# Optimization experiments

Hardware: AMD Instinct MI355X
Metric: run time of the kernel (lower is better)

Reference implementation:

```python
import jax, jax.numpy as jnp
import numpy as np

Q = 8192      # num query tokens
S = 32768     # num support points
E = 131072    # num edges (query<-support neighbor pairs)
D = 256       # token_dim
H = 8         # num_heads
HD = D // H   # head_dim = 32
GEO = 128     # geo mlp_hidden = geo_dim
FFN = 2 * D   # ffn hidden
STAT_IN = 12  # 4 stats * 3 coords
EPS_LN = 1e-5


def gelu(x):
    return jax.nn.gelu(x, approximate=False)  # torch nn.GELU default (erf)


def layernorm(x, g, b):
    m = jnp.mean(x, axis=-1, keepdims=True)
    v = jnp.mean((x - m) ** 2, axis=-1, keepdims=True)
    return (x - m) * jax.lax.rsqrt(v + EPS_LN) * g + b


def setup_inputs() -> dict:
    key = jax.random.key(0)
    ks = jax.random.split(key, 16)
    w = lambda k, shp: jax.random.normal(k, shp, jnp.float32) * 0.02
    return {
        "query_tokens": jax.random.normal(ks[0], (Q, D), jnp.float32),
        "query_pos": jax.random.normal(ks[1], (Q, 3), jnp.float32),
        "support_feats": jax.random.normal(ks[2], (S, D), jnp.float32),
        "support_pos": jax.random.normal(ks[3], (S, 3), jnp.float32),
        "Wq": w(ks[4], (D, D)), "Wk": w(ks[5], (D, D)), "Wv": w(ks[6], (D, D)),
        "Wg": w(ks[7], (GEO, D)),
        "Wo": w(ks[8], (D, D)), "bo": jnp.zeros((D,), jnp.float32),
        "log_tau": jnp.array(0.0, jnp.float32),
        "ln1_g": jnp.ones((D,), jnp.float32), "ln1_b": jnp.zeros((D,), jnp.float32),
        "ln2_g": jnp.ones((D,), jnp.float32), "ln2_b": jnp.zeros((D,), jnp.float32),
        "Wf1": w(ks[9], (D, FFN)), "bf1": jnp.zeros((FFN,), jnp.float32),
        "Wf2": w(ks[10], (FFN, D)), "bf2": jnp.zeros((D,), jnp.float32),
        "Gw1": w(ks[11], (STAT_IN, GEO)), "Gb1": jnp.zeros((GEO,), jnp.float32),
        "Gw2": w(ks[12], (GEO, GEO)), "Gb2": jnp.zeros((GEO,), jnp.float32),
        "q_idx": jnp.sort(jax.random.randint(ks[13], (E,), 0, Q)),
        "s_idx": jax.random.randint(ks[14], (E,), 0, S),
        "num_queries": Q,
    }


def geo_stats(rel, q_idx, num_q):
    # rel: [E,3] relative positions; segmented mean/std/min/max -> [num_q, 12]
    ones = jnp.ones((rel.shape[0], 1), rel.dtype)
    cnt = jnp.maximum(jax.ops.segment_sum(ones, q_idx, num_q), 1.0)  # [Q,1]
    mean = jax.ops.segment_sum(rel, q_idx, num_q) / cnt
    var = jax.ops.segment_sum((rel - mean[q_idx]) ** 2, q_idx, num_q) / cnt
    std = jnp.sqrt(var)
    # torch inits min/max with +/-inf then clamps to [-100,100]; jax segment
    # min/max init with dtype extremes -> same result after clip
    mn = jnp.clip(jax.ops.segment_min(rel, q_idx, num_q), -100.0, 100.0)
    mx = jnp.clip(jax.ops.segment_max(rel, q_idx, num_q), -100.0, 100.0)
    return jnp.concatenate([mean, std, mn, mx], axis=-1)


def reference(query_tokens, query_pos, support_feats, support_pos,
              Wq, Wk, Wv, Wg, Wo, bo, log_tau,
              ln1_g, ln1_b, ln2_g, ln2_b,
              Wf1, bf1, Wf2, bf2, Gw1, Gb1, Gw2, Gb2,
              q_idx, s_idx, num_queries):
    num_q = num_queries
    # ---- statistical geo embedding ----
    rel = support_pos[s_idx] - query_pos[q_idx]                 # [E,3]
    raw = geo_stats(rel, q_idx, num_q)                          # [Q,12]
    geo = gelu(gelu(raw @ Gw1 + Gb1) @ Gw2 + Gb2)               # [Q,GEO]

    # ---- AGNO cross attention (pre-norm) ----
    qt = layernorm(query_tokens, ln1_g, ln1_b)
    Qf = qt @ Wq                                                # [Q,D]
    Kf = support_feats @ Wk                                     # [S,D]
    Vf = support_feats @ Wv                                     # [S,D]
    Gf = geo @ Wg                                               # [Q,D]
    qh = Qf[q_idx].reshape(E, H, HD)
    kh = Kf[s_idx].reshape(E, H, HD)
    vh = Vf[s_idx].reshape(E, H, HD)
    gh = Gf[q_idx].reshape(E, H, HD)
    tau = jnp.exp(log_tau)
    scores = jnp.sum(qh * kh, axis=-1) / (jnp.sqrt(jnp.float32(HD)) * tau)  # [E,H]
    # torch scores_max starts at 0 -> max(0, segment max)
    smax = jnp.maximum(jax.ops.segment_max(scores, q_idx, num_q), 0.0)
    ex = jnp.exp(scores - smax[q_idx])
    ssum = jax.ops.segment_sum(ex, q_idx, num_q)
    alpha = ex / jnp.maximum(ssum[q_idx], 1e-8)                 # [E,H]
    weighted = alpha[..., None] * (vh + gh)                     # [E,H,HD]
    out = jax.ops.segment_sum(weighted, q_idx, num_q)           # [Q,H,HD]
    attn = out.reshape(num_q, D) @ Wo + bo

    # ---- residual + FFN ----
    x = query_tokens + attn
    x = x + gelu(layernorm(x, ln2_g, ln2_b) @ Wf1 + bf1) @ Wf2 + bf2
    return x
```

## Files before the change

kernel.cpp:

```cpp
#include <hip/hip_runtime.h>
#include <math.h>

#define QN 8192
#define SN 32768
#define EN 131072
#define DN 256
#define HN 8
#define HDN 32
#define GEON 128
#define FFNN 512

typedef __attribute__((ext_vector_type(8))) short bf16x8;
typedef __attribute__((ext_vector_type(8))) unsigned short u16x8;
typedef __attribute__((ext_vector_type(4))) unsigned short u16x4;
typedef __attribute__((ext_vector_type(4))) float f32x4;

__device__ __forceinline__ unsigned short f2b(float f) {
  union { float f; unsigned u; } v; v.f = f;
  unsigned u = v.u;
  u += 0x7fffu + ((u >> 16) & 1u);
  return (unsigned short)(u >> 16);
}
__device__ __forceinline__ float b2f(unsigned short h) {
  union { unsigned u; float f; } v; v.u = ((unsigned)h) << 16; return v.f;
}
__device__ __forceinline__ float gelu_f(float x) {
  return 0.5f * x * (1.0f + erff(x * 0.70710678118654752440f));
}

__global__ __launch_bounds__(256) void transpose_weights(
    const float* Wq, const float* Wk, const float* Wv, const float* Wg,
    const float* Wo, const float* Wf1, const float* Wf2,
    unsigned short* WqT, unsigned short* WkvT, unsigned short* WgT,
    unsigned short* WoT, unsigned short* Wf1T, unsigned short* Wf2T) {
  int b = blockIdx.x;
  const float* src; unsigned short* dst; int K, N, tile;
  if (b < 16)       { src = Wq;  dst = WqT;          K = 256; N = 256; tile = b; }
  else if (b < 32)  { src = Wk;  dst = WkvT;         K = 256; N = 256; tile = b - 16; }
  else if (b < 48)  { src = Wv;  dst = WkvT + 65536; K = 256; N = 256; tile = b - 32; }
  else if (b < 56)  { src = Wg;  dst = WgT;          K = 128; N = 256; tile = b - 48; }
  else if (b < 72)  { src = Wo;  dst = WoT;          K = 256; N = 256; tile = b - 56; }
  else if (b < 104) { src = Wf1; dst = Wf1T;         K = 256; N = 512; tile = b - 72; }
  else              { src = Wf2; dst = Wf2T;         K = 512; N = 256; tile = b - 104; }
  int ktiles = K >> 6;
  int k0 = (tile % ktiles) * 64, n0 = (tile / ktiles) * 64;
  __shared__ float ts[64][65];
  int t = threadIdx.x;
  int c4 = (t & 15) * 4;
  int r = t >> 4;
#pragma unroll
  for (int p = 0; p < 4; ++p) {
    int row = p * 16 + r;
    float4 v = *(const float4*)(src + (size_t)(k0 + row) * N + n0 + c4);
    ts[row][c4 + 0] = v.x; ts[row][c4 + 1] = v.y;
    ts[row][c4 + 2] = v.z; ts[row][c4 + 3] = v.w;
  }
  __syncthreads();
#pragma unroll
  for (int p = 0; p < 4; ++p) {
    int n = p * 16 + r;
    ushort4 o;
    o.x = f2b(ts[c4 + 0][n]); o.y = f2b(ts[c4 + 1][n]);
    o.z = f2b(ts[c4 + 2][n]); o.w = f2b(ts[c4 + 3][n]);
    *(ushort4*)(dst + (size_t)(n0 + n) * K + k0 + c4) = o;
  }
}

__global__ __launch_bounds__(256) void seg_offsets(const int* q_idx, int* offs) {
  int i = blockIdx.x * 256 + threadIdx.x;
  if (i > QN) return;
  int lo = 0, hi = EN;
  while (lo < hi) {
    int mid = (lo + hi) >> 1;
    if (q_idx[mid] < i) lo = mid + 1; else hi = mid;
  }
  offs[i] = lo;
}

__global__ __launch_bounds__(256) void geo_stats_kernel(
    const float* qpos, const float* spos, const int* offs, const int* s_idx, float* raw) {
  int q = blockIdx.x * 64 + (threadIdx.x >> 2);
  int sub = threadIdx.x & 3;
  int e0 = offs[q], e1 = offs[q + 1];
  float qx = qpos[q * 3 + 0], qy = qpos[q * 3 + 1], qz = qpos[q * 3 + 2];
  float cnt = 0.f, sx = 0.f, sy = 0.f, sz = 0.f, sxx = 0.f, syy = 0.f, szz = 0.f;
  float mnx = 1e30f, mny = 1e30f, mnz = 1e30f, mxx = -1e30f, mxy = -1e30f, mxz = -1e30f;
  for (int e = e0 + sub; e < e1; e += 4) {
    int s = s_idx[e];
    float rx = spos[s * 3 + 0] - qx;
    float ry = spos[s * 3 + 1] - qy;
    float rz = spos[s * 3 + 2] - qz;
    cnt += 1.f;
    sx += rx; sy += ry; sz += rz;
    sxx += rx * rx; syy += ry * ry; szz += rz * rz;
    mnx = fminf(mnx, rx); mny = fminf(mny, ry); mnz = fminf(mnz, rz);
    mxx = fmaxf(mxx, rx); mxy = fmaxf(mxy, ry); mxz = fmaxf(mxz, rz);
  }
#pragma unroll
  for (int msk = 1; msk <= 2; msk <<= 1) {
    cnt += __shfl_xor(cnt, msk);
    sx += __shfl_xor(sx, msk); sy += __shfl_xor(sy, msk); sz += __shfl_xor(sz, msk);
    sxx += __shfl_xor(sxx, msk); syy += __shfl_xor(syy, msk); szz += __shfl_xor(szz, msk);
    mnx = fminf(mnx, __shfl_xor(mnx, msk));
    mny = fminf(mny, __shfl_xor(mny, msk));
    mnz = fminf(mnz, __shfl_xor(mnz, msk));
    mxx = fmaxf(mxx, __shfl_xor(mxx, msk));
    mxy = fmaxf(mxy, __shfl_xor(mxy, msk));
    mxz = fmaxf(mxz, __shfl_xor(mxz, msk));
  }
  if (sub == 0) {
    float c = fmaxf(cnt, 1.f);
    float mx_ = sx / c, my_ = sy / c, mz_ = sz / c;
    float vx = fmaxf(sxx / c - mx_ * mx_, 0.f);
    float vy = fmaxf(syy / c - my_ * my_, 0.f);
    float vz = fmaxf(szz / c - mz_ * mz_, 0.f);
    float* r = raw + (size_t)q * 12;
    r[0] = mx_; r[1] = my_; r[2] = mz_;
    r[3] = sqrtf(vx); r[4] = sqrtf(vy); r[5] = sqrtf(vz);
    r[6] = fminf(fmaxf(mnx, -100.f), 100.f);
    r[7] = fminf(fmaxf(mny, -100.f), 100.f);
    r[8] = fminf(fmaxf(mnz, -100.f), 100.f);
    r[9] = fminf(fmaxf(mxx, -100.f), 100.f);
    r[10] = fminf(fmaxf(mxy, -100.f), 100.f);
    r[11] = fminf(fmaxf(mxz, -100.f), 100.f);
  }
}

__global__ __launch_bounds__(128) void geo_mlp_kernel(
    const float* raw, const float* Gw1, const float* Gb1,
    const float* Gw2, const float* Gb2, unsigned short* geo_b) {
  int qb = blockIdx.x * 8;
  int j = threadIdx.x;
  __shared__ float rs[8][12];
  __shared__ float h1[8][128];
  if (j < 96) rs[j / 12][j % 12] = raw[(size_t)(qb + j / 12) * 12 + (j % 12)];
  __syncthreads();
  float b1 = Gb1[j];
  float acc[8];
#pragma unroll
  for (int qq = 0; qq < 8; ++qq) acc[qq] = b1;
  for (int i = 0; i < 12; ++i) {
    float w = Gw1[i * GEON + j];
#pragma unroll
    for (int qq = 0; qq < 8; ++qq) acc[qq] += rs[qq][i] * w;
  }
#pragma unroll
  for (int qq = 0; qq < 8; ++qq) h1[qq][j] = gelu_f(acc[qq]);
  __syncthreads();
  float b2 = Gb2[j];
  float acc2[8];
#pragma unroll
  for (int qq = 0; qq < 8; ++qq) acc2[qq] = b2;
  for (int k = 0; k < 128; ++k) {
    float w = Gw2[k * GEON + j];
#pragma unroll
    for (int qq = 0; qq < 8; ++qq) acc2[qq] += h1[qq][k] * w;
  }
#pragma unroll
  for (int qq = 0; qq < 8; ++qq)
    geo_b[(size_t)(qb + qq) * GEON + j] = f2b(gelu_f(acc2[qq]));
}

__global__ __launch_bounds__(256) void ln_kernel(
    const float* x, const float* g, const float* b, unsigned short* out) {
  int row = blockIdx.x * 4 + (threadIdx.x >> 6);
  int lane = threadIdx.x & 63;
  const float* xr = x + (size_t)row * DN;
  float4 v = *(const float4*)(xr + lane * 4);
  float s = v.x + v.y + v.z + v.w;
  float ss = v.x * v.x + v.y * v.y + v.z * v.z + v.w * v.w;
#pragma unroll
  for (int msk = 1; msk <= 32; msk <<= 1) {
    s += __shfl_xor(s, msk);
    ss += __shfl_xor(ss, msk);
  }
  float mean = s * (1.f / 256.f);
  float var = ss * (1.f / 256.f) - mean * mean;
  float rs = 1.0f / sqrtf(var + 1e-5f);
  float4 gg = *(const float4*)(g + lane * 4);
  float4 bb = *(const float4*)(b + lane * 4);
  unsigned short* o = out + (size_t)row * DN + lane * 4;
  o[0] = f2b((v.x - mean) * rs * gg.x + bb.x);
  o[1] = f2b((v.y - mean) * rs * gg.y + bb.y);
  o[2] = f2b((v.z - mean) * rs * gg.z + bb.z);
  o[3] = f2b((v.w - mean) * rs * gg.w + bb.w);
}

__device__ __forceinline__ u16x8* lds_g(unsigned short* base, int row, int col) {
  int g = (col >> 3) ^ (row & 7);
  return reinterpret_cast<u16x8*>(base + row * 256 + g * 8);
}
__global__ __launch_bounds__(256) void kv_gemm(
    const float* A, const unsigned short* BT, unsigned short* KVb) {
  __shared__ unsigned short As[64 * 256];
  __shared__ unsigned short Bs[32 * 256];
  int t = threadIdx.x;
  int bm = blockIdx.x * 64;
  int w = t >> 6, lane = t & 63;
  int quad = lane >> 4, l16 = lane & 15;
  int wr = w >> 1, wc = w & 1;
  int srow = t >> 2, sub = t & 3;
  {
    const float* Ag = A + (size_t)(bm + srow) * 256 + sub * 64;
#pragma unroll
    for (int i = 0; i < 8; ++i) {
      float4 f0 = *(const float4*)(Ag + i * 8);
      float4 f1 = *(const float4*)(Ag + i * 8 + 4);
      u16x8 u;
      u[0] = f2b(f0.x); u[1] = f2b(f0.y); u[2] = f2b(f0.z); u[3] = f2b(f0.w);
      u[4] = f2b(f1.x); u[5] = f2b(f1.y); u[6] = f2b(f1.z); u[7] = f2b(f1.w);
      *lds_g(As, srow, sub * 64 + i * 8) = u;
    }
  }
  int brow = t >> 3, bsub = t & 7;
  for (int ct = 0; ct < 16; ++ct) {
    {
      const unsigned short* Bg = BT + (size_t)(ct * 32 + brow) * 256 + bsub * 32;
#pragma unroll
      for (int i = 0; i < 4; ++i)
        *lds_g(Bs, brow, bsub * 32 + i * 8) = *reinterpret_cast<const u16x8*>(Bg + i * 8);
    }
    __syncthreads();
    f32x4 acc[2];
    acc[0] = (f32x4){0.f, 0.f, 0.f, 0.f};
    acc[1] = (f32x4){0.f, 0.f, 0.f, 0.f};
#pragma unroll
    for (int k = 0; k < 8; ++k) {
      bf16x8 a0 = *reinterpret_cast<bf16x8*>(lds_g(As, wr * 32 + l16, k * 32 + quad * 8));
      bf16x8 a1 = *reinterpret_cast<bf16x8*>(lds_g(As, wr * 32 + 16 + l16, k * 32 + quad * 8));
      bf16x8 b0 = *reinterpret_cast<bf16x8*>(lds_g(Bs, wc * 16 + l16, k * 32 + quad * 8));
      acc[0] = __builtin_amdgcn_mfma_f32_16x16x32_bf16(a0, b0, acc[0], 0, 0, 0);
      acc[1] = __builtin_amdgcn_mfma_f32_16x16x32_bf16(a1, b0, acc[1], 0, 0, 0);
    }
#pragma unroll
    for (int i = 0; i < 2; ++i)
#pragma unroll
      for (int r = 0; r < 4; ++r) {
        int rw = bm + wr * 32 + i * 16 + quad * 4 + r;
        int col = ct * 32 + wc * 16 + l16;
        KVb[(size_t)rw * 512 + col] = f2b(acc[i][r]);
      }
    __syncthreads();
  }
}

template <bool A_FP32, bool COLGRID, bool HAS_BIAS, bool DO_GELU, bool HAS_RESID, bool STORE_F32>
__global__ __launch_bounds__(256) void gemm64(
    const void* Ap, const unsigned short* BT, int M, int N, int K,
    const float* bias, const float* resid, float* outF, unsigned short* outB) {
  __shared__ unsigned short As[64][40];
  __shared__ unsigned short Bs[64][40];
  int t = threadIdx.x;
  int bm = (COLGRID ? blockIdx.x : blockIdx.y) * 64;
  int bn = (COLGRID ? blockIdx.y : blockIdx.x) * 64;
  int w = t >> 6, lane = t & 63;
  int wr = w >> 1, wc = w & 1;
  int quad = lane >> 4, l16 = lane & 15;
  int row = t >> 2, chunk = t & 3;

  f32x4 acc[2][2];
#pragma unroll
  for (int i = 0; i < 2; ++i)
#pragma unroll
    for (int j = 0; j < 2; ++j) acc[i][j] = (f32x4){0.f, 0.f, 0.f, 0.f};

  for (int k0 = 0; k0 < K; k0 += 32) {
    if (A_FP32) {
      const float* Ag = (const float*)Ap + (size_t)(bm + row) * K + k0 + chunk * 8;
      float4 f0 = *(const float4*)Ag;
      float4 f1 = *(const float4*)(Ag + 4);
      u16x8 u;
      u[0] = f2b(f0.x); u[1] = f2b(f0.y); u[2] = f2b(f0.z); u[3] = f2b(f0.w);
      u[4] = f2b(f1.x); u[5] = f2b(f1.y); u[6] = f2b(f1.z); u[7] = f2b(f1.w);
      *reinterpret_cast<u16x8*>(&As[row][chunk * 8]) = u;
    } else {
      const unsigned short* Ag = (const unsigned short*)Ap + (size_t)(bm + row) * K + k0 + chunk * 8;
      *reinterpret_cast<u16x8*>(&As[row][chunk * 8]) = *reinterpret_cast<const u16x8*>(Ag);
    }
    {
      const unsigned short* Bg = BT + (size_t)(bn + row) * K + k0 + chunk * 8;
      *reinterpret_cast<u16x8*>(&Bs[row][chunk * 8]) = *reinterpret_cast<const u16x8*>(Bg);
    }
    __syncthreads();
    bf16x8 a0 = *reinterpret_cast<const bf16x8*>(&As[wr * 32 + l16][quad * 8]);
    bf16x8 a1 = *reinterpret_cast<const bf16x8*>(&As[wr * 32 + 16 + l16][quad * 8]);
    bf16x8 b0 = *reinterpret_cast<const bf16x8*>(&Bs[wc * 32 + l16][quad * 8]);
    bf16x8 b1 = *reinterpret_cast<const bf16x8*>(&Bs[wc * 32 + 16 + l16][quad * 8]);
    acc[0][0] = __builtin_amdgcn_mfma_f32_16x16x32_bf16(a0, b0, acc[0][0], 0, 0, 0);
    acc[0][1] = __builtin_amdgcn_mfma_f32_16x16x32_bf16(a0, b1, acc[0][1], 0, 0, 0);
    acc[1][0] = __builtin_amdgcn_mfma_f32_16x16x32_bf16(a1, b0, acc[1][0], 0, 0, 0);
    acc[1][1] = __builtin_amdgcn_mfma_f32_16x16x32_bf16(a1, b1, acc[1][1], 0, 0, 0);
    __syncthreads();
  }

#pragma unroll
  for (int i = 0; i < 2; ++i)
#pragma unroll
    for (int j = 0; j < 2; ++j) {
      int col = bn + wc * 32 + j * 16 + l16;
      float bv = HAS_BIAS ? bias[col] : 0.f;
#pragma unroll
      for (int r = 0; r < 4; ++r) {
        int rw = bm + wr * 32 + i * 16 + quad * 4 + r;
        float v = acc[i][j][r] + bv;
        if (DO_GELU) v = gelu_f(v);
        if (HAS_RESID) v += resid[(size_t)rw * N + col];
        if (STORE_F32) outF[(size_t)rw * N + col] = v;
        else outB[(size_t)rw * N + col] = f2b(v);
      }
    }
}

__global__ __launch_bounds__(256) void attn_edge_kernel(
    const unsigned short* Qb, const unsigned short* Gfb, const unsigned short* KVb,
    const int* s_idx, const int* offs, const float* log_tau, unsigned short* attn_b) {
  int q = blockIdx.x * 4 + (threadIdx.x >> 6);
  int lane = threadIdx.x & 63;
  int half = lane >> 5;
  int sl = lane & 31;
  int d0 = sl * 8;
  int e0 = offs[q], e1 = offs[q + 1];
  float invs = expf(-log_tau[0]) * 0.17677669529663687f;
  u16x8 qu = *(const u16x8*)(Qb + (size_t)q * DN + d0);
  u16x8 gu = *(const u16x8*)(Gfb + (size_t)q * DN + d0);
  float qf[8], gf[8];
#pragma unroll
  for (int j = 0; j < 8; ++j) { qf[j] = b2f(qu[j]) * invs; gf[j] = b2f(gu[j]); }
  const float NEG = -1e30f;
  float m = -INFINITY, l = 0.f;
  float a[8];
#pragma unroll
  for (int j = 0; j < 8; ++j) a[j] = 0.f;
  for (int e = e0; e < e1; e += 2) {
    int ee = e + half;
    bool valid = ee < e1;
    int s = s_idx[valid ? ee : (e1 - 1)];
    const unsigned short* kr = KVb + (size_t)s * 512 + d0;
    u16x8 ku = *(const u16x8*)kr;
    u16x8 vu = *(const u16x8*)(kr + 256);
    float p = 0.f;
#pragma unroll
    for (int j = 0; j < 8; ++j) p += qf[j] * b2f(ku[j]);
    p += __shfl_xor(p, 1);
    p += __shfl_xor(p, 2);
    if (!valid) p = -INFINITY;
    float mnew = fmaxf(m, p);
    float sc = (m > NEG) ? __expf(m - mnew) : 0.f;
    float we = valid ? __expf(p - mnew) : 0.f;
    l = l * sc + we;
#pragma unroll
    for (int j = 0; j < 8; ++j) a[j] = a[j] * sc + we * (b2f(vu[j]) + gf[j]);
    m = mnew;
  }
  float om = __shfl_xor(m, 32);
  float ol = __shfl_xor(l, 32);
  float M2 = fmaxf(m, om);
  float ws = (m > NEG) ? __expf(m - M2) : 0.f;
  float wo = (om > NEG) ? __expf(om - M2) : 0.f;
  l = l * ws + ol * wo;
#pragma unroll
  for (int j = 0; j < 8; ++j) {
    float oa = __shfl_xor(a[j], 32);
    a[j] = a[j] * ws + oa * wo;
  }
  float M = fmaxf(M2, 0.f);
  float em = (M2 > NEG) ? __expf(M2 - M) : 0.f;
  float denom = fmaxf(l * em, 1e-8f);
  float f = em / denom;
  if (half == 0) {
    u16x8 o;
#pragma unroll
    for (int j = 0; j < 8; ++j) o[j] = f2b(a[j] * f);
    *(u16x8*)(attn_b + (size_t)q * DN + d0) = o;
  }
}

extern "C" void kernel_launch(void* const* d_in, const int* in_sizes, int n_in,
                              void* d_out, int out_size, void* d_ws, size_t ws_size,
                              hipStream_t stream) {
  const float* query_tokens  = (const float*)d_in[0];
  const float* query_pos     = (const float*)d_in[1];
  const float* support_feats = (const float*)d_in[2];
  const float* support_pos   = (const float*)d_in[3];
  const float* Wq  = (const float*)d_in[4];
  const float* Wk  = (const float*)d_in[5];
  const float* Wv  = (const float*)d_in[6];
  const float* Wg  = (const float*)d_in[7];
  const float* Wo  = (const float*)d_in[8];
  const float* bo  = (const float*)d_in[9];
  const float* log_tau = (const float*)d_in[10];
  const float* ln1_g = (const float*)d_in[11];
  const float* ln1_b = (const float*)d_in[12];
  const float* ln2_g = (const float*)d_in[13];
  const float* ln2_b = (const float*)d_in[14];
  const float* Wf1 = (const float*)d_in[15];
  const float* bf1 = (const float*)d_in[16];
  const float* Wf2 = (const float*)d_in[17];
  const float* bf2 = (const float*)d_in[18];
  const float* Gw1 = (const float*)d_in[19];
  const float* Gb1 = (const float*)d_in[20];
  const float* Gw2 = (const float*)d_in[21];
  const float* Gb2 = (const float*)d_in[22];
  const int* q_idx = (const int*)d_in[23];
  const int* s_idx = (const int*)d_in[24];
  float* out = (float*)d_out;

  char* ws = (char*)d_ws;
  size_t off = 0;
  auto alloc = [&](size_t bytes) -> void* {
    void* p = ws + off;
    off = (off + bytes + 255) & ~(size_t)255;
    return p;
  };
  unsigned short* WqT  = (unsigned short*)alloc(65536 * 2);
  unsigned short* WkvT = (unsigned short*)alloc(131072 * 2);
  unsigned short* WgT  = (unsigned short*)alloc(32768 * 2);
  unsigned short* WoT  = (unsigned short*)alloc(65536 * 2);
  unsigned short* Wf1T = (unsigned short*)alloc(131072 * 2);
  unsigned short* Wf2T = (unsigned short*)alloc(131072 * 2);
  int* offs            = (int*)alloc((QN + 1) * 4);
  float* raw           = (float*)alloc((size_t)QN * 12 * 4);
  unsigned short* geo_b = (unsigned short*)alloc((size_t)QN * GEON * 2);
  unsigned short* qt_b  = (unsigned short*)alloc((size_t)QN * DN * 2);
  unsigned short* Qb    = (unsigned short*)alloc((size_t)QN * DN * 2);
  unsigned short* Gf_b  = (unsigned short*)alloc((size_t)QN * DN * 2);
  unsigned short* KVb   = (unsigned short*)alloc((size_t)SN * 512 * 2);
  unsigned short* attn_b = (unsigned short*)alloc((size_t)QN * DN * 2);
  float* x1             = (float*)alloc((size_t)QN * DN * 4);
  unsigned short* z_b   = (unsigned short*)alloc((size_t)QN * DN * 2);
  unsigned short* h_b   = (unsigned short*)alloc((size_t)QN * FFNN * 2);

  transpose_weights<<<136, 256, 0, stream>>>(Wq, Wk, Wv, Wg, Wo, Wf1, Wf2,
                                             WqT, WkvT, WgT, WoT, Wf1T, Wf2T);
  seg_offsets<<<33, 256, 0, stream>>>(q_idx, offs);
  geo_stats_kernel<<<QN / 64, 256, 0, stream>>>(query_pos, support_pos, offs, s_idx, raw);
  geo_mlp_kernel<<<QN / 8, 128, 0, stream>>>(raw, Gw1, Gb1, Gw2, Gb2, geo_b);
  ln_kernel<<<QN / 4, 256, 0, stream>>>(query_tokens, ln1_g, ln1_b, qt_b);
  kv_gemm<<<SN / 64, 256, 0, stream>>>(support_feats, WkvT, KVb);
  gemm64<false, true, false, false, false, false><<<dim3(QN / 64, DN / 64), 256, 0, stream>>>(
      qt_b, WqT, QN, DN, 256, nullptr, nullptr, nullptr, Qb);
  gemm64<false, true, false, false, false, false><<<dim3(QN / 64, DN / 64), 256, 0, stream>>>(
      geo_b, WgT, QN, DN, 128, nullptr, nullptr, nullptr, Gf_b);
  attn_edge_kernel<<<QN / 4, 256, 0, stream>>>(Qb, Gf_b, KVb, s_idx, offs, log_tau, attn_b);
  gemm64<false, true, true, false, true, true><<<dim3(QN / 64, DN / 64), 256, 0, stream>>>(
      attn_b, WoT, QN, DN, 256, bo, query_tokens, x1, nullptr);
  ln_kernel<<<QN / 4, 256, 0, stream>>>(x1, ln2_g, ln2_b, z_b);
  gemm64<false, true, true, true, false, false><<<dim3(QN / 64, FFNN / 64), 256, 0, stream>>>(
      z_b, Wf1T, QN, FFNN, 256, bf1, nullptr, nullptr, h_b);
  gemm64<false, true, true, false, true, true><<<dim3(QN / 64, DN / 64), 256, 0, stream>>>(
      h_b, Wf2T, QN, DN, 512, bf2, x1, out, nullptr);

  (void)in_sizes; (void)n_in; (void)out_size; (void)ws_size;
}
```

Baseline: 250.9 us.

## Fuse prep kernels, merge Q/G GEMMs, fuse Wo GEMM with LayerNorm2

```diff
diff --git a/kernel.cpp b/kernel.cpp
--- a/kernel.cpp
+++ b/kernel.cpp
@@ -28,53 +28,79 @@
   return 0.5f * x * (1.0f + erff(x * 0.70710678118654752440f));
 }
 
-__global__ __launch_bounds__(256) void transpose_weights(
+#define TRB 136
+#define SOB 33
+__global__ __launch_bounds__(256) void prep_kernel(
     const float* Wq, const float* Wk, const float* Wv, const float* Wg,
     const float* Wo, const float* Wf1, const float* Wf2,
     unsigned short* WqT, unsigned short* WkvT, unsigned short* WgT,
-    unsigned short* WoT, unsigned short* Wf1T, unsigned short* Wf2T) {
+    unsigned short* WoT, unsigned short* Wf1T, unsigned short* Wf2T,
+    const int* q_idx, int* offs,
+    const float* x, const float* g, const float* bln, unsigned short* qt_b) {
+  __shared__ float ts[64][65];
   int b = blockIdx.x;
-  const float* src; unsigned short* dst; int K, N, tile;
-  if (b < 16)       { src = Wq;  dst = WqT;          K = 256; N = 256; tile = b; }
-  else if (b < 32)  { src = Wk;  dst = WkvT;         K = 256; N = 256; tile = b - 16; }
-  else if (b < 48)  { src = Wv;  dst = WkvT + 65536; K = 256; N = 256; tile = b - 32; }
-  else if (b < 56)  { src = Wg;  dst = WgT;          K = 128; N = 256; tile = b - 48; }
-  else if (b < 72)  { src = Wo;  dst = WoT;          K = 256; N = 256; tile = b - 56; }
-  else if (b < 104) { src = Wf1; dst = Wf1T;         K = 256; N = 512; tile = b - 72; }
-  else              { src = Wf2; dst = Wf2T;         K = 512; N = 256; tile = b - 104; }
-  int ktiles = K >> 6;
-  int k0 = (tile % ktiles) * 64, n0 = (tile / ktiles) * 64;
-  __shared__ float ts[64][65];
   int t = threadIdx.x;
-  int c4 = (t & 15) * 4;
-  int r = t >> 4;
-#pragma unroll
-  for (int p = 0; p < 4; ++p) {
-    int row = p * 16 + r;
-    float4 v = *(const float4*)(src + (size_t)(k0 + row) * N + n0 + c4);
-    ts[row][c4 + 0] = v.x; ts[row][c4 + 1] = v.y;
-    ts[row][c4 + 2] = v.z; ts[row][c4 + 3] = v.w;
-  }
-  __syncthreads();
-#pragma unroll
-  for (int p = 0; p < 4; ++p) {
-    int n = p * 16 + r;
-    ushort4 o;
-    o.x = f2b(ts[c4 + 0][n]); o.y = f2b(ts[c4 + 1][n]);
-    o.z = f2b(ts[c4 + 2][n]); o.w = f2b(ts[c4 + 3][n]);
-    *(ushort4*)(dst + (size_t)(n0 + n) * K + k0 + c4) = o;
-  }
-}
-
-__global__ __launch_bounds__(256) void seg_offsets(const int* q_idx, int* offs) {
-  int i = blockIdx.x * 256 + threadIdx.x;
-  if (i > QN) return;
-  int lo = 0, hi = EN;
-  while (lo < hi) {
-    int mid = (lo + hi) >> 1;
-    if (q_idx[mid] < i) lo = mid + 1; else hi = mid;
-  }
-  offs[i] = lo;
+  if (b < TRB) {
+    const float* src; unsigned short* dst; int K, N, tile;
+    if (b < 16)       { src = Wq;  dst = WqT;          K = 256; N = 256; tile = b; }
+    else if (b < 32)  { src = Wk;  dst = WkvT;         K = 256; N = 256; tile = b - 16; }
+    else if (b < 48)  { src = Wv;  dst = WkvT + 65536; K = 256; N = 256; tile = b - 32; }
+    else if (b < 56)  { src = Wg;  dst = WgT;          K = 128; N = 256; tile = b - 48; }
+    else if (b < 72)  { src = Wo;  dst = WoT;          K = 256; N = 256; tile = b - 56; }
+    else if (b < 104) { src = Wf1; dst = Wf1T;         K = 256; N = 512; tile = b - 72; }
+    else              { src = Wf2; dst = Wf2T;         K = 512; N = 256; tile = b - 104; }
+    int ktiles = K >> 6;
+    int k0 = (tile % ktiles) * 64, n0 = (tile / ktiles) * 64;
+    int c4 = (t & 15) * 4;
+    int r = t >> 4;
+#pragma unroll
+    for (int p = 0; p < 4; ++p) {
+      int row = p * 16 + r;
+      float4 v = *(const float4*)(src + (size_t)(k0 + row) * N + n0 + c4);
+      ts[row][c4 + 0] = v.x; ts[row][c4 + 1] = v.y;
+      ts[row][c4 + 2] = v.z; ts[row][c4 + 3] = v.w;
+    }
+    __syncthreads();
+#pragma unroll
+    for (int p = 0; p < 4; ++p) {
+      int n = p * 16 + r;
+      ushort4 o;
+      o.x = f2b(ts[c4 + 0][n]); o.y = f2b(ts[c4 + 1][n]);
+      o.z = f2b(ts[c4 + 2][n]); o.w = f2b(ts[c4 + 3][n]);
+      *(ushort4*)(dst + (size_t)(n0 + n) * K + k0 + c4) = o;
+    }
+  } else if (b < TRB + SOB) {
+    int i = (b - TRB) * 256 + t;
+    if (i > QN) return;
+    int lo = 0, hi = EN;
+    while (lo < hi) {
+      int mid = (lo + hi) >> 1;
+      if (q_idx[mid] < i) lo = mid + 1; else hi = mid;
+    }
+    offs[i] = lo;
+  } else {
+    int row = (b - TRB - SOB) * 4 + (t >> 6);
+    int lane = t & 63;
+    const float* xr = x + (size_t)row * DN;
+    float4 v = *(const float4*)(xr + lane * 4);
+    float s = v.x + v.y + v.z + v.w;
+    float ss = v.x * v.x + v.y * v.y + v.z * v.z + v.w * v.w;
+#pragma unroll
+    for (int msk = 1; msk <= 32; msk <<= 1) {
+      s += __shfl_xor(s, msk);
+      ss += __shfl_xor(ss, msk);
+    }
+    float mean = s * (1.f / 256.f);
+    float var = ss * (1.f / 256.f) - mean * mean;
+    float rs = 1.0f / sqrtf(var + 1e-5f);
+    float4 gg = *(const float4*)(g + lane * 4);
+    float4 bb = *(const float4*)(bln + lane * 4);
+    unsigned short* o = qt_b + (size_t)row * DN + lane * 4;
+    o[0] = f2b((v.x - mean) * rs * gg.x + bb.x);
+    o[1] = f2b((v.y - mean) * rs * gg.y + bb.y);
+    o[2] = f2b((v.z - mean) * rs * gg.z + bb.z);
+    o[3] = f2b((v.w - mean) * rs * gg.w + bb.w);
+  }
 }
 
 __global__ __launch_bounds__(256) void geo_stats_kernel(
@@ -126,64 +152,36 @@
   }
 }
 
-__global__ __launch_bounds__(128) void geo_mlp_kernel(
+__global__ __launch_bounds__(256) void geo_mlp_kernel(
     const float* raw, const float* Gw1, const float* Gb1,
     const float* Gw2, const float* Gb2, unsigned short* geo_b) {
-  int qb = blockIdx.x * 8;
-  int j = threadIdx.x;
-  __shared__ float rs[8][12];
-  __shared__ float h1[8][128];
-  if (j < 96) rs[j / 12][j % 12] = raw[(size_t)(qb + j / 12) * 12 + (j % 12)];
-  __syncthreads();
-  float b1 = Gb1[j];
-  float acc[8];
-#pragma unroll
-  for (int qq = 0; qq < 8; ++qq) acc[qq] = b1;
-  for (int i = 0; i < 12; ++i) {
-    float w = Gw1[i * GEON + j];
-#pragma unroll
-    for (int qq = 0; qq < 8; ++qq) acc[qq] += rs[qq][i] * w;
-  }
-#pragma unroll
-  for (int qq = 0; qq < 8; ++qq) h1[qq][j] = gelu_f(acc[qq]);
-  __syncthreads();
-  float b2 = Gb2[j];
-  float acc2[8];
-#pragma unroll
-  for (int qq = 0; qq < 8; ++qq) acc2[qq] = b2;
+  int q = blockIdx.x * 4 + (threadIdx.x >> 6);
+  int lane = threadIdx.x & 63;
+  float rv[12];
+#pragma unroll
+  for (int i = 0; i < 12; ++i) rv[i] = raw[(size_t)q * 12 + i];
+  int k0 = lane * 2;
+  float h[2];
+#pragma unroll
+  for (int kk = 0; kk < 2; ++kk) {
+    float a = Gb1[k0 + kk];
+#pragma unroll
+    for (int i = 0; i < 12; ++i) a += rv[i] * Gw1[i * GEON + k0 + kk];
+    h[kk] = gelu_f(a);
+  }
+  int j0 = lane * 2;
+  float a0 = Gb2[j0], a1 = Gb2[j0 + 1];
+#pragma unroll
   for (int k = 0; k < 128; ++k) {
-    float w = Gw2[k * GEON + j];
-#pragma unroll
-    for (int qq = 0; qq < 8; ++qq) acc2[qq] += h1[qq][k] * w;
-  }
-#pragma unroll
-  for (int qq = 0; qq < 8; ++qq)
-    geo_b[(size_t)(qb + qq) * GEON + j] = f2b(gelu_f(acc2[qq]));
-}
-
-__global__ __launch_bounds__(256) void ln_kernel(
-    const float* x, const float* g, const float* b, unsigned short* out) {
-  int row = blockIdx.x * 4 + (threadIdx.x >> 6);
-  int lane = threadIdx.x & 63;
-  const float* xr = x + (size_t)row * DN;
-  float4 v = *(const float4*)(xr + lane * 4);
-  float s = v.x + v.y + v.z + v.w;
-  float ss = v.x * v.x + v.y * v.y + v.z * v.z + v.w * v.w;
-#pragma unroll
-  for (int msk = 1; msk <= 32; msk <<= 1) {
-    s += __shfl_xor(s, msk);
-    ss += __shfl_xor(ss, msk);
-  }
-  float mean = s * (1.f / 256.f);
-  float var = ss * (1.f / 256.f) - mean * mean;
-  float rs = 1.0f / sqrtf(var + 1e-5f);
-  float4 gg = *(const float4*)(g + lane * 4);
-  float4 bb = *(const float4*)(b + lane * 4);
-  unsigned short* o = out + (size_t)row * DN + lane * 4;
-  o[0] = f2b((v.x - mean) * rs * gg.x + bb.x);
-  o[1] = f2b((v.y - mean) * rs * gg.y + bb.y);
-  o[2] = f2b((v.z - mean) * rs * gg.z + bb.z);
-  o[3] = f2b((v.w - mean) * rs * gg.w + bb.w);
+    float hk = __shfl(h[k & 1], k >> 1);
+    float2 w = *(const float2*)(Gw2 + (size_t)k * GEON + j0);
+    a0 += hk * w.x;
+    a1 += hk * w.y;
+  }
+  ushort2 o;
+  o.x = f2b(gelu_f(a0));
+  o.y = f2b(gelu_f(a1));
+  *(ushort2*)(geo_b + (size_t)q * GEON + j0) = o;
 }
 
 __device__ __forceinline__ u16x8* lds_g(unsigned short* base, int row, int col) {
@@ -244,15 +242,15 @@
   }
 }
 
-template <bool A_FP32, bool COLGRID, bool HAS_BIAS, bool DO_GELU, bool HAS_RESID, bool STORE_F32>
+template <bool HAS_BIAS, bool DO_GELU, bool HAS_RESID, bool STORE_F32>
 __global__ __launch_bounds__(256) void gemm64(
-    const void* Ap, const unsigned short* BT, int M, int N, int K,
+    const unsigned short* A, const unsigned short* BT, int M, int N, int K,
     const float* bias, const float* resid, float* outF, unsigned short* outB) {
   __shared__ unsigned short As[64][40];
   __shared__ unsigned short Bs[64][40];
   int t = threadIdx.x;
-  int bm = (COLGRID ? blockIdx.x : blockIdx.y) * 64;
-  int bn = (COLGRID ? blockIdx.y : blockIdx.x) * 64;
+  int bm = blockIdx.x * 64;
+  int bn = blockIdx.y * 64;
   int w = t >> 6, lane = t & 63;
   int wr = w >> 1, wc = w & 1;
   int quad = lane >> 4, l16 = lane & 15;
@@ -265,16 +263,8 @@
     for (int j = 0; j < 2; ++j) acc[i][j] = (f32x4){0.f, 0.f, 0.f, 0.f};
 
   for (int k0 = 0; k0 < K; k0 += 32) {
-    if (A_FP32) {
-      const float* Ag = (const float*)Ap + (size_t)(bm + row) * K + k0 + chunk * 8;
-      float4 f0 = *(const float4*)Ag;
-      float4 f1 = *(const float4*)(Ag + 4);
-      u16x8 u;
-      u[0] = f2b(f0.x); u[1] = f2b(f0.y); u[2] = f2b(f0.z); u[3] = f2b(f0.w);
-      u[4] = f2b(f1.x); u[5] = f2b(f1.y); u[6] = f2b(f1.z); u[7] = f2b(f1.w);
-      *reinterpret_cast<u16x8*>(&As[row][chunk * 8]) = u;
-    } else {
-      const unsigned short* Ag = (const unsigned short*)Ap + (size_t)(bm + row) * K + k0 + chunk * 8;
+    {
+      const unsigned short* Ag = A + (size_t)(bm + row) * K + k0 + chunk * 8;
       *reinterpret_cast<u16x8*>(&As[row][chunk * 8]) = *reinterpret_cast<const u16x8*>(Ag);
     }
     {
@@ -307,6 +297,58 @@
         if (HAS_RESID) v += resid[(size_t)rw * N + col];
         if (STORE_F32) outF[(size_t)rw * N + col] = v;
         else outB[(size_t)rw * N + col] = f2b(v);
+      }
+    }
+}
+
+__global__ __launch_bounds__(256) void qg_gemm(
+    const unsigned short* qt_b, const unsigned short* WqT,
+    const unsigned short* geo_b, const unsigned short* WgT,
+    unsigned short* Qb, unsigned short* Gf_b) {
+  __shared__ unsigned short As[64][40];
+  __shared__ unsigned short Bs[64][40];
+  int t = threadIdx.x;
+  int by = blockIdx.y;
+  const unsigned short* A; const unsigned short* BT; unsigned short* outB; int K; int bn;
+  if (by < 4) { A = qt_b;  BT = WqT; outB = Qb;   K = 256; bn = by * 64; }
+  else        { A = geo_b; BT = WgT; outB = Gf_b; K = 128; bn = (by - 4) * 64; }
+  int bm = blockIdx.x * 64;
+  int w = t >> 6, lane = t & 63;
+  int wr = w >> 1, wc = w & 1;
+  int quad = lane >> 4, l16 = lane & 15;
+  int row = t >> 2, chunk = t & 3;
+
+  f32x4 acc[2][2];
+#pragma unroll
+  for (int i = 0; i < 2; ++i)
+#pragma unroll
+    for (int j = 0; j < 2; ++j) acc[i][j] = (f32x4){0.f, 0.f, 0.f, 0.f};
+
+  for (int k0 = 0; k0 < K; k0 += 32) {
+    *reinterpret_cast<u16x8*>(&As[row][chunk * 8]) =
+        *reinterpret_cast<const u16x8*>(A + (size_t)(bm + row) * K + k0 + chunk * 8);
+    *reinterpret_cast<u16x8*>(&Bs[row][chunk * 8]) =
+        *reinterpret_cast<const u16x8*>(BT + (size_t)(bn + row) * K + k0 + chunk * 8);
+    __syncthreads();
+    bf16x8 a0 = *reinterpret_cast<const bf16x8*>(&As[wr * 32 + l16][quad * 8]);
+    bf16x8 a1 = *reinterpret_cast<const bf16x8*>(&As[wr * 32 + 16 + l16][quad * 8]);
+    bf16x8 b0 = *reinterpret_cast<const bf16x8*>(&Bs[wc * 32 + l16][quad * 8]);
+    bf16x8 b1 = *reinterpret_cast<const bf16x8*>(&Bs[wc * 32 + 16 + l16][quad * 8]);
+    acc[0][0] = __builtin_amdgcn_mfma_f32_16x16x32_bf16(a0, b0, acc[0][0], 0, 0, 0);
+    acc[0][1] = __builtin_amdgcn_mfma_f32_16x16x32_bf16(a0, b1, acc[0][1], 0, 0, 0);
+    acc[1][0] = __builtin_amdgcn_mfma_f32_16x16x32_bf16(a1, b0, acc[1][0], 0, 0, 0);
+    acc[1][1] = __builtin_amdgcn_mfma_f32_16x16x32_bf16(a1, b1, acc[1][1], 0, 0, 0);
+    __syncthreads();
+  }
+#pragma unroll
+  for (int i = 0; i < 2; ++i)
+#pragma unroll
+    for (int j = 0; j < 2; ++j) {
+      int col = bn + wc * 32 + j * 16 + l16;
+#pragma unroll
+      for (int r = 0; r < 4; ++r) {
+        int rw = bm + wr * 32 + i * 16 + quad * 4 + r;
+        outB[(size_t)rw * DN + col] = f2b(acc[i][j][r]);
       }
     }
 }
@@ -355,13 +397,13 @@
   float om = __shfl_xor(m, 32);
   float ol = __shfl_xor(l, 32);
   float M2 = fmaxf(m, om);
-  float ws = (m > NEG) ? __expf(m - M2) : 0.f;
+  float wsc = (m > NEG) ? __expf(m - M2) : 0.f;
   float wo = (om > NEG) ? __expf(om - M2) : 0.f;
-  l = l * ws + ol * wo;
+  l = l * wsc + ol * wo;
 #pragma unroll
   for (int j = 0; j < 8; ++j) {
     float oa = __shfl_xor(a[j], 32);
-    a[j] = a[j] * ws + oa * wo;
+    a[j] = a[j] * wsc + oa * wo;
   }
   float M = fmaxf(M2, 0.f);
   float em = (M2 > NEG) ? __expf(M2 - M) : 0.f;
@@ -373,6 +415,111 @@
     for (int j = 0; j < 8; ++j) o[j] = f2b(a[j] * f);
     *(u16x8*)(attn_b + (size_t)q * DN + d0) = o;
   }
+}
+
+__global__ __launch_bounds__(256) void wo_ln2_kernel(
+    const unsigned short* A, const unsigned short* WoT, const float* bo,
+    const float* resid, const float* g2, const float* b2,
+    float* x1, unsigned short* z_b) {
+  __shared__ unsigned short As[64][40];
+  __shared__ unsigned short Bs[256][40];
+  __shared__ float prt[64][4][2];
+  __shared__ float mrs[64][2];
+  int t = threadIdx.x;
+  int bm = blockIdx.x * 64;
+  int w = t >> 6, lane = t & 63;
+  int quad = lane >> 4, l16 = lane & 15;
+  int arow = t >> 2, achunk = t & 3;
+
+  f32x4 acc[4][4];
+#pragma unroll
+  for (int i = 0; i < 4; ++i)
+#pragma unroll
+    for (int j = 0; j < 4; ++j) acc[i][j] = (f32x4){0.f, 0.f, 0.f, 0.f};
+
+  for (int k0 = 0; k0 < 256; k0 += 32) {
+    *reinterpret_cast<u16x8*>(&As[arow][achunk * 8]) =
+        *reinterpret_cast<const u16x8*>(A + (size_t)(bm + arow) * 256 + k0 + achunk * 8);
+    const unsigned short* Bg = WoT + (size_t)t * 256 + k0;
+    *reinterpret_cast<u16x8*>(&Bs[t][0]) = *reinterpret_cast<const u16x8*>(Bg);
+    *reinterpret_cast<u16x8*>(&Bs[t][8]) = *reinterpret_cast<const u16x8*>(Bg + 8);
+    *reinterpret_cast<u16x8*>(&Bs[t][16]) = *reinterpret_cast<const u16x8*>(Bg + 16);
+    *reinterpret_cast<u16x8*>(&Bs[t][24]) = *reinterpret_cast<const u16x8*>(Bg + 24);
+    __syncthreads();
+    bf16x8 bfr[4];
+#pragma unroll
+    for (int ct = 0; ct < 4; ++ct)
+      bfr[ct] = *reinterpret_cast<const bf16x8*>(&Bs[w * 64 + ct * 16 + l16][quad * 8]);
+#pragma unroll
+    for (int rt = 0; rt < 4; ++rt) {
+      bf16x8 afr = *reinterpret_cast<const bf16x8*>(&As[rt * 16 + l16][quad * 8]);
+#pragma unroll
+      for (int ct = 0; ct < 4; ++ct)
+        acc[rt][ct] = __builtin_amdgcn_mfma_f32_16x16x32_bf16(afr, bfr[ct], acc[rt][ct], 0, 0, 0);
+    }
+    __syncthreads();
+  }
+
+  float bov[4], g2v[4], b2v[4];
+#pragma unroll
+  for (int ct = 0; ct < 4; ++ct) {
+    int col = w * 64 + ct * 16 + l16;
+    bov[ct] = bo[col]; g2v[ct] = g2[col]; b2v[ct] = b2[col];
+  }
+#pragma unroll
+  for (int rt = 0; rt < 4; ++rt)
+#pragma unroll
+    for (int ct = 0; ct < 4; ++ct) {
+      int col = w * 64 + ct * 16 + l16;
+#pragma unroll
+      for (int r = 0; r < 4; ++r) {
+        int rw = bm + rt * 16 + quad * 4 + r;
+        float v = acc[rt][ct][r] + bov[ct] + resid[(size_t)rw * DN + col];
+        x1[(size_t)rw * DN + col] = v;
+        acc[rt][ct][r] = v;
+      }
+    }
+#pragma unroll
+  for (int rt = 0; rt < 4; ++rt)
+#pragma unroll
+    for (int r = 0; r < 4; ++r) {
+      float s = acc[rt][0][r] + acc[rt][1][r] + acc[rt][2][r] + acc[rt][3][r];
+      float ss = acc[rt][0][r] * acc[rt][0][r] + acc[rt][1][r] * acc[rt][1][r] +
+                 acc[rt][2][r] * acc[rt][2][r] + acc[rt][3][r] * acc[rt][3][r];
+#pragma unroll
+      for (int msk = 1; msk <= 8; msk <<= 1) {
+        s += __shfl_xor(s, msk);
+        ss += __shfl_xor(ss, msk);
+      }
+      if (l16 == 0) {
+        int row = rt * 16 + quad * 4 + r;
+        prt[row][w][0] = s;
+        prt[row][w][1] = ss;
+      }
+    }
+  __syncthreads();
+  if (t < 64) {
+    float s = prt[t][0][0] + prt[t][1][0] + prt[t][2][0] + prt[t][3][0];
+    float ss = prt[t][0][1] + prt[t][1][1] + prt[t][2][1] + prt[t][3][1];
+    float mean = s * (1.f / 256.f);
+    float var = ss * (1.f / 256.f) - mean * mean;
+    mrs[t][0] = mean;
+    mrs[t][1] = 1.0f / sqrtf(var + 1e-5f);
+  }
+  __syncthreads();
+#pragma unroll
+  for (int rt = 0; rt < 4; ++rt)
+#pragma unroll
+    for (int ct = 0; ct < 4; ++ct) {
+      int col = w * 64 + ct * 16 + l16;
+#pragma unroll
+      for (int r = 0; r < 4; ++r) {
+        int row = rt * 16 + quad * 4 + r;
+        int rw = bm + row;
+        float z = (acc[rt][ct][r] - mrs[row][0]) * mrs[row][1] * g2v[ct] + b2v[ct];
+        z_b[(size_t)rw * DN + col] = f2b(z);
+      }
+    }
 }
 
 extern "C" void kernel_launch(void* const* d_in, const int* in_sizes, int n_in,
@@ -430,24 +577,19 @@
   unsigned short* z_b   = (unsigned short*)alloc((size_t)QN * DN * 2);
   unsigned short* h_b   = (unsigned short*)alloc((size_t)QN * FFNN * 2);
 
-  transpose_weights<<<136, 256, 0, stream>>>(Wq, Wk, Wv, Wg, Wo, Wf1, Wf2,
-                                             WqT, WkvT, WgT, WoT, Wf1T, Wf2T);
-  seg_offsets<<<33, 256, 0, stream>>>(q_idx, offs);
+  prep_kernel<<<TRB + SOB + QN / 4, 256, 0, stream>>>(
+      Wq, Wk, Wv, Wg, Wo, Wf1, Wf2, WqT, WkvT, WgT, WoT, Wf1T, Wf2T,
+      q_idx, offs, query_tokens, ln1_g, ln1_b, qt_b);
   geo_stats_kernel<<<QN / 64, 256, 0, stream>>>(query_pos, support_pos, offs, s_idx, raw);
-  geo_mlp_kernel<<<QN / 8, 128, 0, stream>>>(raw, Gw1, Gb1, Gw2, Gb2, geo_b);
-  ln_kernel<<<QN / 4, 256, 0, stream>>>(query_tokens, ln1_g, ln1_b, qt_b);
+  geo_mlp_kernel<<<QN / 4, 256, 0, stream>>>(raw, Gw1, Gb1, Gw2, Gb2, geo_b);
   kv_gemm<<<SN / 64, 256, 0, stream>>>(support_feats, WkvT, KVb);
-  gemm64<false, true, false, false, false, false><<<dim3(QN / 64, DN / 64), 256, 0, stream>>>(
-      qt_b, WqT, QN, DN, 256, nullptr, nullptr, nullptr, Qb);
-  gemm64<false, true, false, false, false, false><<<dim3(QN / 64, DN / 64), 256, 0, stream>>>(
-      geo_b, WgT, QN, DN, 128, nullptr, nullptr, nullptr, Gf_b);
+  qg_gemm<<<dim3(QN / 64, 8), 256, 0, stream>>>(qt_b, WqT, geo_b, WgT, Qb, Gf_b);
   attn_edge_kernel<<<QN / 4, 256, 0, stream>>>(Qb, Gf_b, KVb, s_idx, offs, log_tau, attn_b);
-  gemm64<false, true, true, false, true, true><<<dim3(QN / 64, DN / 64), 256, 0, stream>>>(
-      attn_b, WoT, QN, DN, 256, bo, query_tokens, x1, nullptr);
-  ln_kernel<<<QN / 4, 256, 0, stream>>>(x1, ln2_g, ln2_b, z_b);
-  gemm64<false, true, true, true, false, false><<<dim3(QN / 64, FFNN / 64), 256, 0, stream>>>(
+  wo_ln2_kernel<<<QN / 64, 256, 0, stream>>>(attn_b, WoT, bo, query_tokens,
+                                             ln2_g, ln2_b, x1, z_b);
+  gemm64<true, true, false, false><<<dim3(QN / 64, FFNN / 64), 256, 0, stream>>>(
       z_b, Wf1T, QN, FFNN, 256, bf1, nullptr, nullptr, h_b);
-  gemm64<false, true, true, false, true, true><<<dim3(QN / 64, DN / 64), 256, 0, stream>>>(
+  gemm64<true, false, true, true><<<dim3(QN / 64, DN / 64), 256, 0, stream>>>(
       h_b, Wf2T, QN, DN, 512, bf2, x1, out, nullptr);
 
   (void)in_sizes; (void)n_in; (void)out_size; (void)ws_size;
```

Measured after the change: 279.4 us. +11.4%, slower.
